# Kernel tuning notes

Measured on AMD Instinct MI355X. Metric: run time of the kernel, lower is better.

The kernel has to match this reference:

```python
import jax, jax.numpy as jnp
import numpy as np

N_NODES = 100000
N_EDGES = 3200000
DIN, DHID, DOUT = 128, 128, 128


def setup_inputs() -> dict:
    key = jax.random.key(0)
    ks = jax.random.split(key, 8)
    x = jax.random.normal(ks[0], (N_NODES, DIN), dtype=jnp.float32)
    edge_index = jax.random.randint(ks[1], (2, N_EDGES), 0, N_NODES, dtype=jnp.int32)
    def glorot(k, fan_in, fan_out):
        s = jnp.sqrt(6.0 / (fan_in + fan_out)).astype(jnp.float32)
        return jax.random.uniform(k, (fan_in, fan_out), jnp.float32, -s, s)
    return {
        "x": x,
        "edge_index": edge_index,
        "w1": glorot(ks[2], DIN, DHID), "b1": jnp.zeros((DHID,), jnp.float32),
        "w2": glorot(ks[3], DHID, DHID), "b2": jnp.zeros((DHID,), jnp.float32),
        "w3": glorot(ks[4], DHID, DOUT), "b3": jnp.zeros((DOUT,), jnp.float32),
    }


def reference(x, edge_index, w1, b1, w2, b2, w3, b3):
    n = x.shape[0]
    # GCN normalization with self-loops (PyG gcn_norm, edge_weight = 1)
    loop = jnp.arange(n, dtype=edge_index.dtype)
    src = jnp.concatenate([edge_index[0], loop])  # [E+N]
    dst = jnp.concatenate([edge_index[1], loop])  # [E+N]
    deg = jax.ops.segment_sum(jnp.ones_like(dst, dtype=x.dtype), dst, num_segments=n)
    dinv = jnp.where(deg > 0, jax.lax.rsqrt(deg), 0.0)
    norm = dinv[src] * dinv[dst]  # [E+N]

    def gcn_conv(h, w, b):
        h = h @ w  # [N, dout]
        msg = norm[:, None] * h[src]  # gather + scale, [E+N, dout]
        agg = jax.ops.segment_sum(msg, dst, num_segments=n)  # scatter-add
        return agg + b

    h = jax.nn.relu(gcn_conv(x, w1, b1))
    h = jax.nn.relu(gcn_conv(h, w2, b2))  # dropout p=0 / eval: no-op
    h = gcn_conv(h, w3, b3)
    return jnp.sum(h, axis=0, keepdims=True) / h.shape[0]  # [1, DOUT]
```

## Files before the change

kernel.cpp:

```cpp
#include <hip/hip_runtime.h>

#define D 128
#define BSH 8
#define CAP 10240
#define CH 8192

typedef unsigned short ushort_t;
typedef unsigned int uint_t;
typedef unsigned char uchar_t;

typedef __attribute__((ext_vector_type(8))) short frag_ab;
typedef __attribute__((ext_vector_type(4))) float frag_cd;
typedef __attribute__((ext_vector_type(2))) float float2v;

union frag_u { ushort_t u[8]; frag_ab v; };


__device__ __forceinline__ float bf2f(ushort_t u) {
    union { uint_t i; float f; } v; v.i = ((uint_t)u) << 16; return v.f;
}
__device__ __forceinline__ ushort_t f2bf(float f) {
    union { float f; uint_t i; } v; v.f = f;
    uint_t u = v.i;
    u += 0x7fffu + ((u >> 16) & 1u);
    return (ushort_t)(u >> 16);
}

__launch_bounds__(512)
__global__ void k_bin(const int* __restrict__ src, const int* __restrict__ dst,
                      int* __restrict__ curA, int* __restrict__ curB,
                      uint_t* __restrict__ binA, uint_t* __restrict__ binB,
                      int E, int nb) {
    __shared__ int hA[512], hB[512], bA[512], bB[512];
    int tx = threadIdx.x;
    for (int i = tx; i < nb; i += 512) { hA[i] = 0; hB[i] = 0; }
    __syncthreads();

    int e0 = blockIdx.x * CH;
    int e1 = min(e0 + CH, E);

    for (int e = e0 + tx; e < e1; e += 512) {
        atomicAdd(&hA[dst[e] >> BSH], 1);
        atomicAdd(&hB[src[e] >> BSH], 1);
    }
    __syncthreads();
    for (int i = tx; i < nb; i += 512) {
        bA[i] = hA[i] ? atomicAdd(&curA[i], hA[i]) : 0;
        bB[i] = hB[i] ? atomicAdd(&curB[i], hB[i]) : 0;
        hA[i] = 0; hB[i] = 0;
    }
    __syncthreads();
    for (int e = e0 + tx; e < e1; e += 512) {
        int s = src[e], d = dst[e];
        int ka = d >> BSH, kb = s >> BSH;
        int pa = bA[ka] + atomicAdd(&hA[ka], 1);
        int pb = bB[kb] + atomicAdd(&hB[kb], 1);
        if (pa < CAP) binA[(size_t)ka * CAP + pa] = ((uint_t)s << 8) | (uint_t)(d & 255);
        if (pb < CAP) binB[(size_t)kb * CAP + pb] = ((uint_t)d << 8) | (uint_t)(s & 255);
    }
}

__launch_bounds__(1024)
__global__ void k_csr(const uint_t* __restrict__ binA, const int* __restrict__ curA,
                      float* __restrict__ dinv, int* __restrict__ row_beg,
                      int* __restrict__ row_end, int* __restrict__ csr_src, int N) {
    __shared__ int hist[256];
    __shared__ int scan[256];
    int b = blockIdx.x;
    int tx = threadIdx.x;
    int cnt = min(curA[b], CAP);
    const uint_t* eb = binA + (size_t)b * CAP;

    if (tx < 256) hist[tx] = 0;
    __syncthreads();
    for (int e = tx; e < cnt; e += 1024)
        atomicAdd(&hist[eb[e] & 255u], 1);
    __syncthreads();
    int v = 0;
    if (tx < 256) { v = hist[tx]; scan[tx] = v; }
    __syncthreads();
    for (int dd = 1; dd < 256; dd <<= 1) {
        int t = 0;
        if (tx < 256 && tx >= dd) t = scan[tx - dd];
        __syncthreads();
        if (tx < 256) scan[tx] += t;
        __syncthreads();
    }
    if (tx < 256) {
        int my_excl = scan[tx] - v;
        int node = b * 256 + tx;
        if (node < N) {
            dinv[node] = rsqrtf((float)(v + 1));
            row_beg[node] = b * CAP + my_excl;
            row_end[node] = b * CAP + my_excl + v;
        }
        hist[tx] = my_excl;
    }
    __syncthreads();
    for (int e = tx; e < cnt; e += 1024) {
        uint_t pk = eb[e];
        int pos = b * CAP + atomicAdd(&hist[pk & 255u], 1);
        csr_src[pos] = (int)(pk >> 8);
    }
}

__global__ void k_wpack(const float* __restrict__ W1, const float* __restrict__ W2,
                        ushort_t* __restrict__ h1, ushort_t* __restrict__ l1,
                        ushort_t* __restrict__ h2, ushort_t* __restrict__ l2,
                        const float* __restrict__ b1, const float* __restrict__ b2,
                        float* __restrict__ bp1, float* __restrict__ bp2) {
    if (blockIdx.x == 128) {
        int p = threadIdx.x;
        if (p < 128) {
            int c = (p & 7) * 16 + (p >> 3);
            bp1[p] = b1[c];
            bp2[p] = b2[c];
        }
        return;
    }
    int gid = blockIdx.x * 256 + threadIdx.x;
    int which = gid >> 14;
    int idx = gid & 16383;
    int k = idx >> 7, n = idx & 127;
    float w = which ? W2[(((k & 7) * 16) + (k >> 3)) * 128 + n] : W1[idx];
    ushort_t h = f2bf(w);
    ushort_t l = f2bf(w - bf2f(h));
    int c = k >> 5, quad = (k >> 3) & 3, jj = k & 7;
    int j = n >> 4, l16 = n & 15;
    int lane = quad * 16 + l16;
    int dest = ((c * 8 + j) * 64 + lane) * 8 + jj;
    if (which) { h2[dest] = h; l2[dest] = l; }
    else       { h1[dest] = h; l1[dest] = l; }
}

template <int IN_F32>
__launch_bounds__(256)
__global__ void gemm_mfma(const void* __restrict__ Av, const ushort_t* __restrict__ Whi,
                          const ushort_t* __restrict__ Wlo, const float* __restrict__ dinv,
                          uchar_t* __restrict__ C8, int nrows) {
    int wave = threadIdx.x >> 6;
    int lane = threadIdx.x & 63;
    int quad = lane >> 4, l16 = lane & 15;
    int base = blockIdx.x * 128 + wave * 32;

    frag_cd acc[2][8];
#pragma unroll
    for (int rt = 0; rt < 2; rt++)
#pragma unroll
        for (int j = 0; j < 8; j++) acc[rt][j] = (frag_cd)0.f;

    const ushort_t* Ab = (const ushort_t*)Av;
    const float* Af = (const float*)Av;

#pragma unroll
    for (int c = 0; c < 4; c++) {
        frag_ab afrag[2];
        int koff = c * 32 + quad * 8;
#pragma unroll
        for (int rt = 0; rt < 2; rt++) {
            int row = min(base + rt * 16 + l16, nrows - 1);
            if (IN_F32) {
                const float* ap = Af + (size_t)row * D + koff;
                float4 a0 = *(const float4*)ap;
                float4 a1 = *(const float4*)(ap + 4);
                frag_u fu;
                fu.u[0] = f2bf(a0.x); fu.u[1] = f2bf(a0.y);
                fu.u[2] = f2bf(a0.z); fu.u[3] = f2bf(a0.w);
                fu.u[4] = f2bf(a1.x); fu.u[5] = f2bf(a1.y);
                fu.u[6] = f2bf(a1.z); fu.u[7] = f2bf(a1.w);
                afrag[rt] = fu.v;
            } else {
                afrag[rt] = *(const frag_ab*)(Ab + (size_t)row * D + koff);
            }
        }
#pragma unroll
        for (int j = 0; j < 8; j++) {
            frag_ab bh = *(const frag_ab*)(Whi + (((c * 8 + j) * 64 + lane) * 8));
            frag_ab bl = *(const frag_ab*)(Wlo + (((c * 8 + j) * 64 + lane) * 8));
#pragma unroll
            for (int rt = 0; rt < 2; rt++) {
                acc[rt][j] = __builtin_amdgcn_mfma_f32_16x16x32_bf16(afrag[rt], bh,
                                                                     acc[rt][j], 0, 0, 0);
                acc[rt][j] = __builtin_amdgcn_mfma_f32_16x16x32_bf16(afrag[rt], bl,
                                                                     acc[rt][j], 0, 0, 0);
            }
        }
    }

#pragma unroll
    for (int rt = 0; rt < 2; rt++) {
        int rbase = base + rt * 16 + quad * 4;
#pragma unroll
        for (int reg = 0; reg < 4; reg++) {
            int row = rbase + reg;
            if (row < nrows) {
                float dv = dinv[row];
                uint_t d0 = (uint_t)__builtin_amdgcn_cvt_pk_fp8_f32(
                    acc[rt][0][reg] * dv, acc[rt][1][reg] * dv, 0, false);
                d0 = (uint_t)__builtin_amdgcn_cvt_pk_fp8_f32(
                    acc[rt][2][reg] * dv, acc[rt][3][reg] * dv, (int)d0, true);
                uint_t d1 = (uint_t)__builtin_amdgcn_cvt_pk_fp8_f32(
                    acc[rt][4][reg] * dv, acc[rt][5][reg] * dv, 0, false);
                d1 = (uint_t)__builtin_amdgcn_cvt_pk_fp8_f32(
                    acc[rt][6][reg] * dv, acc[rt][7][reg] * dv, (int)d1, true);
                uint2 o; o.x = d0; o.y = d1;
                *(uint2*)(C8 + (size_t)row * D + l16 * 8) = o;
            }
        }
    }
}

__launch_bounds__(256)
__global__ void agg8(const uint_t* __restrict__ t8, const int* __restrict__ csr_src,
                     const int* __restrict__ row_beg, const int* __restrict__ row_end,
                     const float* __restrict__ dinv, const float* __restrict__ bias,
                     uint_t* __restrict__ out, int n, int do_relu) {
    int node = blockIdx.x * 4 + (threadIdx.x >> 6);
    if (node >= n) return;
    int lane = threadIdx.x & 63;
    int eh = lane >> 5;
    uint_t cl = (uint_t)(lane & 31);

    int beg = row_beg[node];
    int deg = row_end[node] - beg;
    float dn = dinv[node];

    float2v accA = {0.f, 0.f}, accB = {0.f, 0.f};

    if (eh == 0) {
        uint_t w = t8[(uint_t)node * 32u + cl];
        accA = __builtin_amdgcn_cvt_pk_f32_fp8(w, false);
        accB = __builtin_amdgcn_cvt_pk_f32_fp8(w, true);
    }

    int h0 = (deg + 1) >> 1;
    int e = beg + (eh ? h0 : 0);
    int eend = beg + (eh ? deg : h0);
    for (; e + 7 < eend; e += 8) {
        uint4 sa, sb;
        __builtin_memcpy(&sa, csr_src + e, 16);
        __builtin_memcpy(&sb, csr_src + e + 4, 16);
        uint_t w0 = t8[sa.x * 32u + cl];
        uint_t w1 = t8[sa.y * 32u + cl];
        uint_t w2 = t8[sa.z * 32u + cl];
        uint_t w3 = t8[sa.w * 32u + cl];
        uint_t w4 = t8[sb.x * 32u + cl];
        uint_t w5 = t8[sb.y * 32u + cl];
        uint_t w6 = t8[sb.z * 32u + cl];
        uint_t w7 = t8[sb.w * 32u + cl];
        accA += __builtin_amdgcn_cvt_pk_f32_fp8(w0, false);
        accB += __builtin_amdgcn_cvt_pk_f32_fp8(w0, true);
        accA += __builtin_amdgcn_cvt_pk_f32_fp8(w1, false);
        accB += __builtin_amdgcn_cvt_pk_f32_fp8(w1, true);
        accA += __builtin_amdgcn_cvt_pk_f32_fp8(w2, false);
        accB += __builtin_amdgcn_cvt_pk_f32_fp8(w2, true);
        accA += __builtin_amdgcn_cvt_pk_f32_fp8(w3, false);
        accB += __builtin_amdgcn_cvt_pk_f32_fp8(w3, true);
        accA += __builtin_amdgcn_cvt_pk_f32_fp8(w4, false);
        accB += __builtin_amdgcn_cvt_pk_f32_fp8(w4, true);
        accA += __builtin_amdgcn_cvt_pk_f32_fp8(w5, false);
        accB += __builtin_amdgcn_cvt_pk_f32_fp8(w5, true);
        accA += __builtin_amdgcn_cvt_pk_f32_fp8(w6, false);
        accB += __builtin_amdgcn_cvt_pk_f32_fp8(w6, true);
        accA += __builtin_amdgcn_cvt_pk_f32_fp8(w7, false);
        accB += __builtin_amdgcn_cvt_pk_f32_fp8(w7, true);
    }
    for (; e + 3 < eend; e += 4) {
        uint4 ss;
        __builtin_memcpy(&ss, csr_src + e, 16);
        uint_t w0 = t8[ss.x * 32u + cl];
        uint_t w1 = t8[ss.y * 32u + cl];
        uint_t w2 = t8[ss.z * 32u + cl];
        uint_t w3 = t8[ss.w * 32u + cl];
        accA += __builtin_amdgcn_cvt_pk_f32_fp8(w0, false);
        accB += __builtin_amdgcn_cvt_pk_f32_fp8(w0, true);
        accA += __builtin_amdgcn_cvt_pk_f32_fp8(w1, false);
        accB += __builtin_amdgcn_cvt_pk_f32_fp8(w1, true);
        accA += __builtin_amdgcn_cvt_pk_f32_fp8(w2, false);
        accB += __builtin_amdgcn_cvt_pk_f32_fp8(w2, true);
        accA += __builtin_amdgcn_cvt_pk_f32_fp8(w3, false);
        accB += __builtin_amdgcn_cvt_pk_f32_fp8(w3, true);
    }
    for (; e < eend; ++e) {
        uint_t s = (uint_t)csr_src[e];
        uint_t w = t8[s * 32u + cl];
        accA += __builtin_amdgcn_cvt_pk_f32_fp8(w, false);
        accB += __builtin_amdgcn_cvt_pk_f32_fp8(w, true);
    }

    float a0 = accA.x, a1 = accA.y, a2 = accB.x, a3 = accB.y;
    a0 += __shfl(a0, lane ^ 32, 64);
    a1 += __shfl(a1, lane ^ 32, 64);
    a2 += __shfl(a2, lane ^ 32, 64);
    a3 += __shfl(a3, lane ^ 32, 64);

    if (eh == 0) {
        float4 bb = ((const float4*)bias)[cl];
        float o0 = dn * a0 + bb.x;
        float o1 = dn * a1 + bb.y;
        float o2 = dn * a2 + bb.z;
        float o3 = dn * a3 + bb.w;
        if (do_relu) {
            o0 = fmaxf(o0, 0.f); o1 = fmaxf(o1, 0.f);
            o2 = fmaxf(o2, 0.f); o3 = fmaxf(o3, 0.f);
        }
        uint2 ow;
        ow.x = (uint_t)f2bf(o0) | ((uint_t)f2bf(o1) << 16);
        ow.y = (uint_t)f2bf(o2) | ((uint_t)f2bf(o3) << 16);
        ((uint2*)out)[(size_t)node * 32 + cl] = ow;
    }
}

__launch_bounds__(512)
__global__ void wreduce(const ushort_t* __restrict__ h, const uint_t* __restrict__ binB,
                        const int* __restrict__ curB, const float* __restrict__ dinv,
                        float* __restrict__ v, int n) {
    __shared__ float owacc[256];
    __shared__ float s[512];
    int b = blockIdx.x;
    int tx = threadIdx.x;
    if (tx < 256) owacc[tx] = 0.f;
    __syncthreads();
    int cnt = min(curB[b], CAP);
    const uint_t* eb = binB + (size_t)b * CAP;
    for (int e = tx; e < cnt; e += 512) {
        uint_t pk = eb[e];
        atomicAdd(&owacc[pk & 255u], dinv[pk >> 8]);
    }
    __syncthreads();

    int c = tx & 127;
    int rg = tx >> 7;
    int base = b * 256;
    int lim = min(base + 256, n);
    float acc = 0.f;
    for (int r = base + rg; r < lim; r += 4) {
        float dv = dinv[r];
        float cv = dv * (dv + owacc[r - base]);
        acc += cv * bf2f(h[(size_t)r * D + c]);
    }
    s[tx] = acc;
    __syncthreads();
    if (tx < 128)
        atomicAdd(&v[c], (s[tx] + s[tx + 128]) + (s[tx + 256] + s[tx + 384]));
}

__global__ void finalize(const float* __restrict__ v, const float* __restrict__ w3,
                         const float* __restrict__ b3, float* __restrict__ out, float invn) {
    __shared__ float sv[D];
    int j = threadIdx.x;
    sv[j] = v[j];
    __syncthreads();
    float acc = 0.f;
    for (int k = 0; k < D; k++) {
        int p = (k & 15) * 8 + (k >> 4);
        acc += sv[p] * w3[(size_t)k * D + j];
    }
    out[j] = acc * invn + b3[j];
}

extern "C" void kernel_launch(void* const* d_in, const int* in_sizes, int n_in,
                              void* d_out, int out_size, void* d_ws, size_t ws_size,
                              hipStream_t stream) {
    const float* x   = (const float*)d_in[0];
    const int*   ei  = (const int*)d_in[1];
    const float* w1  = (const float*)d_in[2];
    const float* b1  = (const float*)d_in[3];
    const float* w2  = (const float*)d_in[4];
    const float* b2  = (const float*)d_in[5];
    const float* w3  = (const float*)d_in[6];
    const float* b3  = (const float*)d_in[7];
    float* out = (float*)d_out;

    const int N = in_sizes[0] / D;
    const int E = in_sizes[1] / 2;
    const int* src = ei;
    const int* dst = ei + E;
    const int nb = (N + 255) >> 8;

    char* p = (char*)d_ws;
    auto alloc = [&](size_t bytes) -> char* {
        char* r = p;
        p += (bytes + 255) & ~(size_t)255;
        return r;
    };
    char*     zbeg     = p;
    int*      curA     = (int*)alloc(512 * 4);
    int*      curB     = (int*)alloc(512 * 4);
    float*    v        = (float*)alloc((size_t)D * 4);
    char*     zend     = p;
    float*    dinv     = (float*)alloc((size_t)N * 4);
    int*      row_beg  = (int*)alloc((size_t)N * 4);
    int*      row_end  = (int*)alloc((size_t)N * 4);
    ushort_t* wp1h     = (ushort_t*)alloc(16384 * 2);
    ushort_t* wp1l     = (ushort_t*)alloc(16384 * 2);
    ushort_t* wp2h     = (ushort_t*)alloc(16384 * 2);
    ushort_t* wp2l     = (ushort_t*)alloc(16384 * 2);
    float*    bp1      = (float*)alloc(D * 4);
    float*    bp2      = (float*)alloc(D * 4);
    uint_t*   binA     = (uint_t*)alloc((size_t)nb * CAP * 4);
    uint_t*   binB     = (uint_t*)alloc((size_t)nb * CAP * 4);
    int*      csr_src  = (int*)alloc((size_t)nb * CAP * 4);
    ushort_t* bufH     = (ushort_t*)alloc((size_t)N * D * 2);
    uint_t*   buf8     = (uint_t*)alloc((size_t)N * 32 * 4);
    (void)ws_size;

    const int gG = (N + 127) / 128;

    hipMemsetAsync(zbeg, 0, (size_t)(zend - zbeg), stream);

    k_wpack<<<129, 256, 0, stream>>>(w1, w2, wp1h, wp1l, wp2h, wp2l, b1, b2, bp1, bp2);

    k_bin<<<(E + CH - 1) / CH, 512, 0, stream>>>(src, dst, curA, curB, binA, binB, E, nb);
    k_csr<<<nb, 1024, 0, stream>>>(binA, curA, dinv, row_beg, row_end, csr_src, N);

    gemm_mfma<1><<<gG, 256, 0, stream>>>(x, wp1h, wp1l, dinv, (uchar_t*)buf8, N);
    agg8<<<(N + 3) / 4, 256, 0, stream>>>(buf8, csr_src, row_beg, row_end, dinv, bp1,
                                          (uint_t*)bufH, N, 1);
    gemm_mfma<0><<<gG, 256, 0, stream>>>(bufH, wp2h, wp2l, dinv, (uchar_t*)buf8, N);
    agg8<<<(N + 3) / 4, 256, 0, stream>>>(buf8, csr_src, row_beg, row_end, dinv, bp2,
                                          (uint_t*)bufH, N, 1);
    wreduce<<<nb, 512, 0, stream>>>(bufH, binB, curB, dinv, v, N);
    finalize<<<1, D, 0, stream>>>(v, w3, b3, out, 1.0f / (float)N);
}
```

Baseline: 423.7 us.

## Split fp8 feature table into four column quarters for cache-resident aggregation

The GEMM now writes its fp8 output as four separate column-quarter planes of 32 bytes per row. The aggregation kernel launches four blocks per node group, one per quarter, with 8 lanes per edge and 8 edges in flight per wave. Each gather pass then touches a 3.2MB table instead of 12.8MB, which is meant to raise L2/MALL hit rates on random neighbour gathers. In exchange, CSR indices are read four times, each gather is only a 32-byte segment, and tail edges are masked with redundant loads.

```diff
diff --git a/kernel.cpp b/kernel.cpp
--- a/kernel.cpp
+++ b/kernel.cpp
@@ -137,7 +137,7 @@
 __launch_bounds__(256)
 __global__ void gemm_mfma(const void* __restrict__ Av, const ushort_t* __restrict__ Whi,
                           const ushort_t* __restrict__ Wlo, const float* __restrict__ dinv,
-                          uchar_t* __restrict__ C8, int nrows) {
+                          uint_t* __restrict__ C32, int nrows, int qs ) {
     int wave = threadIdx.x >> 6;
     int lane = threadIdx.x & 63;
     int quad = lane >> 4, l16 = lane & 15;
@@ -187,6 +187,7 @@
         }
     }
 
+    uint_t* qbase = C32 + (size_t)(l16 >> 2) * (size_t)qs + (l16 & 3) * 2;
 #pragma unroll
     for (int rt = 0; rt < 2; rt++) {
         int rbase = base + rt * 16 + quad * 4;
@@ -204,7 +205,7 @@
                 d1 = (uint_t)__builtin_amdgcn_cvt_pk_fp8_f32(
                     acc[rt][6][reg] * dv, acc[rt][7][reg] * dv, (int)d1, true);
                 uint2 o; o.x = d0; o.y = d1;
-                *(uint2*)(C8 + (size_t)row * D + l16 * 8) = o;
+                *(uint2*)(qbase + (size_t)row * 8) = o;
             }
         }
     }
@@ -214,92 +215,57 @@
 __global__ void agg8(const uint_t* __restrict__ t8, const int* __restrict__ csr_src,
                      const int* __restrict__ row_beg, const int* __restrict__ row_end,
                      const float* __restrict__ dinv, const float* __restrict__ bias,
-                     uint_t* __restrict__ out, int n, int do_relu) {
-    int node = blockIdx.x * 4 + (threadIdx.x >> 6);
+                     uint_t* __restrict__ out, int n, int do_relu, int bpq, int qs) {
+    int q = blockIdx.x / bpq;
+    int node = (blockIdx.x - q * bpq) * 4 + (threadIdx.x >> 6);
     if (node >= n) return;
     int lane = threadIdx.x & 63;
-    int eh = lane >> 5;
-    uint_t cl = (uint_t)(lane & 31);
+    int g = lane >> 3;
+    uint_t cl = (uint_t)(lane & 7);
+
+    const uint_t* tq = t8 + (size_t)q * (size_t)qs;
 
     int beg = row_beg[node];
-    int deg = row_end[node] - beg;
+    int end = row_end[node];
     float dn = dinv[node];
 
     float2v accA = {0.f, 0.f}, accB = {0.f, 0.f};
 
-    if (eh == 0) {
-        uint_t w = t8[(uint_t)node * 32u + cl];
-        accA = __builtin_amdgcn_cvt_pk_f32_fp8(w, false);
-        accB = __builtin_amdgcn_cvt_pk_f32_fp8(w, true);
-    }
-
-    int h0 = (deg + 1) >> 1;
-    int e = beg + (eh ? h0 : 0);
-    int eend = beg + (eh ? deg : h0);
-    for (; e + 7 < eend; e += 8) {
-        uint4 sa, sb;
-        __builtin_memcpy(&sa, csr_src + e, 16);
-        __builtin_memcpy(&sb, csr_src + e + 4, 16);
-        uint_t w0 = t8[sa.x * 32u + cl];
-        uint_t w1 = t8[sa.y * 32u + cl];
-        uint_t w2 = t8[sa.z * 32u + cl];
-        uint_t w3 = t8[sa.w * 32u + cl];
-        uint_t w4 = t8[sb.x * 32u + cl];
-        uint_t w5 = t8[sb.y * 32u + cl];
-        uint_t w6 = t8[sb.z * 32u + cl];
-        uint_t w7 = t8[sb.w * 32u + cl];
+    for (int eb = beg; eb < end; eb += 16) {
+        int e0 = eb + g;
+        int e1 = eb + 8 + g;
+        int i0 = min(e0, end - 1);
+        int i1 = min(e1, end - 1);
+        uint_t s0 = (uint_t)csr_src[i0];
+        uint_t s1 = (uint_t)csr_src[i1];
+        uint_t w0 = tq[s0 * 8u + cl];
+        uint_t w1 = tq[s1 * 8u + cl];
+        w0 = (e0 < end) ? w0 : 0u;
+        w1 = (e1 < end) ? w1 : 0u;
         accA += __builtin_amdgcn_cvt_pk_f32_fp8(w0, false);
         accB += __builtin_amdgcn_cvt_pk_f32_fp8(w0, true);
         accA += __builtin_amdgcn_cvt_pk_f32_fp8(w1, false);
         accB += __builtin_amdgcn_cvt_pk_f32_fp8(w1, true);
-        accA += __builtin_amdgcn_cvt_pk_f32_fp8(w2, false);
-        accB += __builtin_amdgcn_cvt_pk_f32_fp8(w2, true);
-        accA += __builtin_amdgcn_cvt_pk_f32_fp8(w3, false);
-        accB += __builtin_amdgcn_cvt_pk_f32_fp8(w3, true);
-        accA += __builtin_amdgcn_cvt_pk_f32_fp8(w4, false);
-        accB += __builtin_amdgcn_cvt_pk_f32_fp8(w4, true);
-        accA += __builtin_amdgcn_cvt_pk_f32_fp8(w5, false);
-        accB += __builtin_amdgcn_cvt_pk_f32_fp8(w5, true);
-        accA += __builtin_amdgcn_cvt_pk_f32_fp8(w6, false);
-        accB += __builtin_amdgcn_cvt_pk_f32_fp8(w6, true);
-        accA += __builtin_amdgcn_cvt_pk_f32_fp8(w7, false);
-        accB += __builtin_amdgcn_cvt_pk_f32_fp8(w7, true);
-    }
-    for (; e + 3 < eend; e += 4) {
-        uint4 ss;
-        __builtin_memcpy(&ss, csr_src + e, 16);
-        uint_t w0 = t8[ss.x * 32u + cl];
-        uint_t w1 = t8[ss.y * 32u + cl];
-        uint_t w2 = t8[ss.z * 32u + cl];
-        uint_t w3 = t8[ss.w * 32u + cl];
-        accA += __builtin_amdgcn_cvt_pk_f32_fp8(w0, false);
-        accB += __builtin_amdgcn_cvt_pk_f32_fp8(w0, true);
-        accA += __builtin_amdgcn_cvt_pk_f32_fp8(w1, false);
-        accB += __builtin_amdgcn_cvt_pk_f32_fp8(w1, true);
-        accA += __builtin_amdgcn_cvt_pk_f32_fp8(w2, false);
-        accB += __builtin_amdgcn_cvt_pk_f32_fp8(w2, true);
-        accA += __builtin_amdgcn_cvt_pk_f32_fp8(w3, false);
-        accB += __builtin_amdgcn_cvt_pk_f32_fp8(w3, true);
-    }
-    for (; e < eend; ++e) {
-        uint_t s = (uint_t)csr_src[e];
-        uint_t w = t8[s * 32u + cl];
-        accA += __builtin_amdgcn_cvt_pk_f32_fp8(w, false);
-        accB += __builtin_amdgcn_cvt_pk_f32_fp8(w, true);
     }
 
     float a0 = accA.x, a1 = accA.y, a2 = accB.x, a3 = accB.y;
-    a0 += __shfl(a0, lane ^ 32, 64);
-    a1 += __shfl(a1, lane ^ 32, 64);
-    a2 += __shfl(a2, lane ^ 32, 64);
-    a3 += __shfl(a3, lane ^ 32, 64);
-
-    if (eh == 0) {
-        float4 bb = ((const float4*)bias)[cl];
-        float o0 = dn * a0 + bb.x;
-        float o1 = dn * a1 + bb.y;
-        float o2 = dn * a2 + bb.z;
-        float o3 = dn * a3 + bb.w;
+#pragma unroll
+    for (int m = 8; m <= 32; m <<= 1) {
+        a0 += __shfl(a0, lane ^ m, 64);
+        a1 += __shfl(a1, lane ^ m, 64);
+        a2 += __shfl(a2, lane ^ m, 64);
+        a3 += __shfl(a3, lane ^ m, 64);
+    }
+
+    if (g == 0) {
+        uint_t ws = tq[(uint_t)node * 8u + cl];
+        float2v slo = __builtin_amdgcn_cvt_pk_f32_fp8(ws, false);
+        float2v shi = __builtin_amdgcn_cvt_pk_f32_fp8(ws, true);
+        float4 bb = ((const float4*)bias)[q * 8 + (int)cl];
+        float o0 = dn * (a0 + slo.x) + bb.x;
+        float o1 = dn * (a1 + slo.y) + bb.y;
+        float o2 = dn * (a2 + shi.x) + bb.z;
+        float o3 = dn * (a3 + shi.y) + bb.w;
         if (do_relu) {
             o0 = fmaxf(o0, 0.f); o1 = fmaxf(o1, 0.f);
             o2 = fmaxf(o2, 0.f); o3 = fmaxf(o3, 0.f);
@@ -307,7 +273,7 @@
         uint2 ow;
         ow.x = (uint_t)f2bf(o0) | ((uint_t)f2bf(o1) << 16);
         ow.y = (uint_t)f2bf(o2) | ((uint_t)f2bf(o3) << 16);
-        ((uint2*)out)[(size_t)node * 32 + cl] = ow;
+        *(uint2*)(out + (size_t)node * 64 + q * 16 + cl * 2) = ow;
     }
 }
 
@@ -405,7 +371,9 @@
     uint_t*   buf8     = (uint_t*)alloc((size_t)N * 32 * 4);
     (void)ws_size;
 
-    const int gG = (N + 127) / 128;
+    const int gG  = (N + 127) / 128;
+    const int bpq = (N + 3) / 4;
+    const int qs  = N * 8;
 
     hipMemsetAsync(zbeg, 0, (size_t)(zend - zbeg), stream);
 
@@ -414,12 +382,12 @@
     k_bin<<<(E + CH - 1) / CH, 512, 0, stream>>>(src, dst, curA, curB, binA, binB, E, nb);
     k_csr<<<nb, 1024, 0, stream>>>(binA, curA, dinv, row_beg, row_end, csr_src, N);
 
-    gemm_mfma<1><<<gG, 256, 0, stream>>>(x, wp1h, wp1l, dinv, (uchar_t*)buf8, N);
-    agg8<<<(N + 3) / 4, 256, 0, stream>>>(buf8, csr_src, row_beg, row_end, dinv, bp1,
-                                          (uint_t*)bufH, N, 1);
-    gemm_mfma<0><<<gG, 256, 0, stream>>>(bufH, wp2h, wp2l, dinv, (uchar_t*)buf8, N);
-    agg8<<<(N + 3) / 4, 256, 0, stream>>>(buf8, csr_src, row_beg, row_end, dinv, bp2,
-                                          (uint_t*)bufH, N, 1);
+    gemm_mfma<1><<<gG, 256, 0, stream>>>(x, wp1h, wp1l, dinv, buf8, N, qs);
+    agg8<<<4 * bpq, 256, 0, stream>>>(buf8, csr_src, row_beg, row_end, dinv, bp1,
+                                      (uint_t*)bufH, N, 1, bpq, qs);
+    gemm_mfma<0><<<gG, 256, 0, stream>>>(bufH, wp2h, wp2l, dinv, buf8, N, qs);
+    agg8<<<4 * bpq, 256, 0, stream>>>(buf8, csr_src, row_beg, row_end, dinv, bp2,
+                                      (uint_t*)bufH, N, 1, bpq, qs);
     wreduce<<<nb, 512, 0, stream>>>(bufH, binB, curB, dinv, v, N);
     finalize<<<1, D, 0, stream>>>(v, w3, b3, out, 1.0f / (float)N);
 }
```

New measurement: 600.9 us. 41.8% more time.
